# Performance work log

Hardware: AMD Instinct MI355X
Metric: run time of the kernel (lower is better)

The kernel has to match this reference:

```python
import jax, jax.numpy as jnp
import numpy as np

E = 768
H = 12
D = E // H  # 64


def setup_inputs() -> dict:
    key = jax.random.key(0)
    ks = jax.random.split(key, 12)
    B, S = 4, 2048
    scale = 1.0 / np.sqrt(E)
    inp = {
        "q": jax.random.normal(ks[0], (B, S, E), jnp.float32),
        "k": jax.random.normal(ks[1], (B, S, E), jnp.float32),
        "v": jax.random.normal(ks[2], (B, S, E), jnp.float32),
        "mask": jax.random.randint(ks[3], (B, S), 0, 2, jnp.int32),
        "Wq": jax.random.normal(ks[4], (E, E), jnp.float32) * scale,
        "bq": jnp.zeros((E,), jnp.float32),
        "Wk": jax.random.normal(ks[5], (E, E), jnp.float32) * scale,
        "bk": jnp.zeros((E,), jnp.float32),
        "Wv": jax.random.normal(ks[6], (E, E), jnp.float32) * scale,
        "bv": jnp.zeros((E,), jnp.float32),
        "Wo": jax.random.normal(ks[7], (E, E), jnp.float32) * scale,
        "bo": jnp.zeros((E,), jnp.float32),
    }
    return inp


def reference(q, k, v, mask, Wq, bq, Wk, bk, Wv, bv, Wo, bo):
    B, Sq, _ = q.shape
    Sk = k.shape[1]
    # QKV projections, split into heads: [B, H, S, D]
    qh = (q @ Wq + bq).reshape(B, Sq, H, D).transpose(0, 2, 1, 3)
    kh = (k @ Wk + bk).reshape(B, Sk, H, D).transpose(0, 2, 1, 3)
    vh = (v @ Wv + bv).reshape(B, Sk, H, D).transpose(0, 2, 1, 3)
    scores = jnp.einsum("bhqd,bhkd->bhqk", qh, kh) / jnp.sqrt(jnp.float32(D))
    # enc=True padding-mask path: positions where mask==0 get -1e9 added
    bias = jnp.where(mask == 0, jnp.float32(-1e9), jnp.float32(0.0))  # [B, Sk]
    scores = scores + bias[:, None, None, :]
    weights = jax.nn.softmax(scores, axis=-1)
    # dropout is identity in eval mode
    ctx = jnp.einsum("bhqk,bhkd->bqhd", weights, vh).reshape(B, Sq, E)
    return ctx @ Wo + bo
```

## Files before the change

kernel.cpp:

```cpp
#include <hip/hip_runtime.h>
#include <hip/hip_bf16.h>
#include <stdint.h>


typedef __bf16 bf16x8 __attribute__((ext_vector_type(8)));
typedef __bf16 bf16x4 __attribute__((ext_vector_type(4)));
typedef float floatx4 __attribute__((ext_vector_type(4)));

#define MFMA_BF16(a, b, c) __builtin_amdgcn_mfma_f32_16x16x32_bf16(a, b, c, 0, 0, 0)


__device__ __forceinline__ void glds16(const __bf16* g, __bf16* l) {
  __builtin_amdgcn_global_load_lds(
      (const __attribute__((address_space(1))) unsigned int*)g,
      (__attribute__((address_space(3))) unsigned int*)l, 16, 0, 0);
}

__global__ __launch_bounds__(256) void prep_transpose(
    const float* __restrict__ W0, const float* __restrict__ W1,
    const float* __restrict__ W2, const float* __restrict__ W3,
    __bf16* __restrict__ T0, __bf16* __restrict__ T1,
    __bf16* __restrict__ T2, __bf16* __restrict__ T3) {
  const int z = blockIdx.z;
  const float* W = (z == 0) ? W0 : (z == 1) ? W1 : (z == 2) ? W2 : W3;
  __bf16* T = (z == 0) ? T0 : (z == 1) ? T1 : (z == 2) ? T2 : T3;
  __shared__ float t[32][33];
  const int tx = threadIdx.x & 31, ty = threadIdx.x >> 5;
  const int kb = blockIdx.x * 32, nb = blockIdx.y * 32;
#pragma unroll
  for (int j = 0; j < 4; ++j)
    t[ty + j * 8][tx] = W[(size_t)(kb + ty + j * 8) * 768 + nb + tx];
  __syncthreads();
#pragma unroll
  for (int j = 0; j < 4; ++j)
    T[(size_t)(nb + ty + j * 8) * 768 + kb + tx] = (__bf16)t[tx][ty + j * 8];
}

__global__ __launch_bounds__(256) void qkv_gemm(
    const __bf16* __restrict__ Wtq, const __bf16* __restrict__ Wtk,
    const __bf16* __restrict__ Wtv, const float* __restrict__ Xq,
    const float* __restrict__ Xk, const float* __restrict__ Xv,
    const float* __restrict__ bq, const float* __restrict__ bk,
    const float* __restrict__ bv, __bf16* __restrict__ Qh,
    __bf16* __restrict__ Kh, __bf16* __restrict__ Vt) {
  __shared__ __align__(16) __bf16 As[128 * 32];
  __shared__ __align__(16) __bf16 Bs[128 * 32];
  const int gid = blockIdx.x + 6 * blockIdx.y + 384 * blockIdx.z;
  const int swz = (gid & 7) * 144 + (gid >> 3);
  const int z = swz / 384;
  const int rem = swz - z * 384;
  const int by = rem / 6;
  const int bx = rem - by * 6;

  const __bf16* Aop = (z == 0) ? Wtq : (z == 1) ? Wtk : Wtv;
  const float* Bop = (z == 0) ? Xq : (z == 1) ? Xk : Xv;
  const float* bias = (z == 0) ? bq : (z == 1) ? bk : bv;
  __bf16* Dst = (z == 0) ? Qh : (z == 1) ? Kh : Vt;
  const int m0 = bx * 128, n0 = by * 128;

  const int tid = threadIdx.x, lane = tid & 63, w = tid >> 6;
  const int quad = lane >> 4, l16 = lane & 15;
  const int wm = (w >> 1) * 64, wn = (w & 1) * 64;

  const int garow = w * 32 + (lane >> 2);
  const int gacol = (lane & 3) * 8;
  const __bf16* gA = Aop + (size_t)(m0 + garow) * 768 + gacol;
  __bf16* lA = As + w * 1024;
  const int brow = tid >> 3, bcol = (tid & 7) * 4;

  floatx4 acc[4][4] = {};

  for (int k0 = 0; k0 < 768; k0 += 32) {
    __syncthreads();
    glds16(gA, lA);
    glds16(gA + (size_t)16 * 768, lA + 512);
    gA += 32;
    float4 f[4];
#pragma unroll
    for (int j = 0; j < 4; ++j)
      f[j] = *(const float4*)&Bop[(size_t)(n0 + brow + 32 * j) * 768 + k0 + bcol];
#pragma unroll
    for (int j = 0; j < 4; ++j) {
      bf16x4 pv;
      pv[0] = (__bf16)f[j].x; pv[1] = (__bf16)f[j].y;
      pv[2] = (__bf16)f[j].z; pv[3] = (__bf16)f[j].w;
      *(bf16x4*)&Bs[(brow + 32 * j) * 32 + bcol] = pv;
    }
    __syncthreads();
    bf16x8 af[4], bfr[4];
#pragma unroll
    for (int t = 0; t < 4; ++t) {
      af[t] = *(const bf16x8*)&As[(wm + t * 16 + l16) * 32 + quad * 8];
      bfr[t] = *(const bf16x8*)&Bs[(wn + t * 16 + l16) * 32 + quad * 8];
    }
#pragma unroll
    for (int mt = 0; mt < 4; ++mt)
#pragma unroll
      for (int nt = 0; nt < 4; ++nt)
        acc[mt][nt] = MFMA_BF16(af[mt], bfr[nt], acc[mt][nt]);
  }

#pragma unroll
  for (int mt = 0; mt < 4; ++mt) {
    const int e = m0 + wm + mt * 16 + quad * 4;
    const float4 b4 = *(const float4*)&bias[e];
    const int h = e >> 6, d = e & 63;
#pragma unroll
    for (int nt = 0; nt < 4; ++nt) {
      const int s = n0 + wn + nt * 16 + l16;
      const int bb = s >> 11, sr = s & 2047;
      const float v0 = acc[mt][nt][0] + b4.x;
      const float v1 = acc[mt][nt][1] + b4.y;
      const float v2 = acc[mt][nt][2] + b4.z;
      const float v3 = acc[mt][nt][3] + b4.w;
      if (z < 2) {
        bf16x4 pv;
        pv[0] = (__bf16)v0; pv[1] = (__bf16)v1; pv[2] = (__bf16)v2; pv[3] = (__bf16)v3;
        const int col = (z == 0) ? d : ((((d >> 3) ^ (sr & 7)) << 3) | (d & 7));
        *(bf16x4*)&Dst[((size_t)(bb * 12 + h) * 2048 + sr) * 64 + col] = pv;
      } else {
        const size_t rowbase = ((size_t)(bb * 12 + h) * 64 + d) * 2048;
        const int shi = sr & ~63, sblk = (sr >> 3) & 7, soff = sr & 7;
        Dst[rowbase + 0 * 2048 + shi + (((sblk ^ ((d + 0) & 7))) << 3) + soff] = (__bf16)v0;
        Dst[rowbase + 1 * 2048 + shi + (((sblk ^ ((d + 1) & 7))) << 3) + soff] = (__bf16)v1;
        Dst[rowbase + 2 * 2048 + shi + (((sblk ^ ((d + 2) & 7))) << 3) + soff] = (__bf16)v2;
        Dst[rowbase + 3 * 2048 + shi + (((sblk ^ ((d + 3) & 7))) << 3) + soff] = (__bf16)v3;
      }
    }
  }
}

__global__ __launch_bounds__(256) void out_gemm(const __bf16* __restrict__ Wto,
                                                const __bf16* __restrict__ Ctx,
                                                const float* __restrict__ bo,
                                                float* __restrict__ Out) {
  __shared__ __align__(16) __bf16 As[128 * 32];
  __shared__ __align__(16) __bf16 Bs[128 * 32];
  const int gid = blockIdx.x + 6 * blockIdx.y;
  const int swz = (gid & 7) * 48 + (gid >> 3);
  const int by = swz / 6;
  const int bx = swz - by * 6;
  const int m0 = bx * 128, n0 = by * 128;
  const int tid = threadIdx.x, lane = tid & 63, w = tid >> 6;
  const int quad = lane >> 4, l16 = lane & 15;
  const int wm = (w >> 1) * 64, wn = (w & 1) * 64;

  const int grow = w * 32 + (lane >> 2);
  const int gcol = (lane & 3) * 8;
  const __bf16* gA = Wto + (size_t)(m0 + grow) * 768 + gcol;
  const __bf16* gB = Ctx + (size_t)(n0 + grow) * 768 + gcol;
  __bf16* lA = As + w * 1024;
  __bf16* lB = Bs + w * 1024;

  floatx4 acc[4][4] = {};
  for (int k0 = 0; k0 < 768; k0 += 32) {
    __syncthreads();
    glds16(gA, lA);
    glds16(gA + (size_t)16 * 768, lA + 512);
    glds16(gB, lB);
    glds16(gB + (size_t)16 * 768, lB + 512);
    gA += 32;
    gB += 32;
    __syncthreads();
    bf16x8 af[4], bfr[4];
#pragma unroll
    for (int t = 0; t < 4; ++t) {
      af[t] = *(const bf16x8*)&As[(wm + t * 16 + l16) * 32 + quad * 8];
      bfr[t] = *(const bf16x8*)&Bs[(wn + t * 16 + l16) * 32 + quad * 8];
    }
#pragma unroll
    for (int mt = 0; mt < 4; ++mt)
#pragma unroll
      for (int nt = 0; nt < 4; ++nt)
        acc[mt][nt] = MFMA_BF16(af[mt], bfr[nt], acc[mt][nt]);
  }

#pragma unroll
  for (int mt = 0; mt < 4; ++mt) {
    const int e = m0 + wm + mt * 16 + quad * 4;
    const float4 b4 = *(const float4*)&bo[e];
#pragma unroll
    for (int nt = 0; nt < 4; ++nt) {
      const int s = n0 + wn + nt * 16 + l16;
      float4 r;
      r.x = acc[mt][nt][0] + b4.x;
      r.y = acc[mt][nt][1] + b4.y;
      r.z = acc[mt][nt][2] + b4.z;
      r.w = acc[mt][nt][3] + b4.w;
      *(float4*)&Out[(size_t)s * 768 + e] = r;
    }
  }
}

__global__ __launch_bounds__(256) void attn_kernel(
    const __bf16* __restrict__ Qh, const __bf16* __restrict__ Kh,
    const __bf16* __restrict__ Vt, const int* __restrict__ mask,
    __bf16* __restrict__ ctx) {
  const int lid = blockIdx.x + 16 * blockIdx.y;
  const int swz = (lid & 7) * 96 + (lid >> 3);
  const int qx = swz & 15, bh = swz >> 4;
  const int b = bh / 12, h = bh - b * 12;
  const int tid = threadIdx.x, lane = tid & 63, w = tid >> 6;
  const int quad = lane >> 4, l16 = lane & 15;
  const int q0 = qx * 128 + w * 32;

  __shared__ __align__(16) __bf16 Ks[2][64 * 64];
  __shared__ __align__(16) __bf16 Vs[2][64 * 64];
  __shared__ __align__(16) __bf16 Plds[4][32][72];

  const __bf16* Qbase = Qh + (size_t)bh * 2048 * 64;
  const __bf16* Kbase = Kh + (size_t)bh * 2048 * 64;
  const __bf16* Vbase = Vt + (size_t)bh * 64 * 2048;
  const int* maskB = mask + b * 2048;

  bf16x8 bqf[2][2];
#pragma unroll
  for (int qt = 0; qt < 2; ++qt)
#pragma unroll
    for (int c = 0; c < 2; ++c)
      bqf[qt][c] =
          *(const bf16x8*)&Qbase[(size_t)(q0 + qt * 16 + l16) * 64 + c * 32 + quad * 8];

  const int r0 = (w * 2) * 8 + (lane >> 3);
  const int r1 = (w * 2 + 1) * 8 + (lane >> 3);
  const int scol = (lane & 7) * 8;
  const int d0 = (w * 2) * 512;
  const int d1 = (w * 2 + 1) * 512;
  const int col0 = (quad ^ (l16 & 7)) * 8;

  glds16(&Kbase[(size_t)r0 * 64 + scol], &Ks[0][d0]);
  glds16(&Kbase[(size_t)r1 * 64 + scol], &Ks[0][d1]);
  glds16(&Vbase[(size_t)r0 * 2048 + scol], &Vs[0][d0]);
  glds16(&Vbase[(size_t)r1 * 2048 + scol], &Vs[0][d1]);

  floatx4 o[4][2] = {};
  float rS[2] = {0.0f, 0.0f};
  const float SC = 0.18033688011112042f;

  for (int it = 0; it < 32; ++it) {
    const int kt = it * 64;
    const int cur = it & 1;
    const int nxt = cur ^ 1;
    const int nkt = (kt + 64) & 2047;

    __syncthreads();

    glds16(&Kbase[(size_t)(nkt + r0) * 64 + scol], &Ks[nxt][d0]);
    glds16(&Kbase[(size_t)(nkt + r1) * 64 + scol], &Ks[nxt][d1]);
    glds16(&Vbase[(size_t)r0 * 2048 + nkt + scol], &Vs[nxt][d0]);
    glds16(&Vbase[(size_t)r1 * 2048 + nkt + scol], &Vs[nxt][d1]);

    int4 mk[4];
#pragma unroll
    for (int t = 0; t < 4; ++t) mk[t] = *(const int4*)&maskB[kt + t * 16 + quad * 4];

    floatx4 sc[4][2];
#pragma unroll
    for (int t = 0; t < 4; ++t) {
      bf16x8 ak0 = *(const bf16x8*)&Ks[cur][(t * 16 + l16) * 64 + col0];
      bf16x8 ak1 = *(const bf16x8*)&Ks[cur][(t * 16 + l16) * 64 + (col0 ^ 32)];
#pragma unroll
      for (int qt = 0; qt < 2; ++qt) {
        floatx4 zz = {};
        zz = MFMA_BF16(ak0, bqf[qt][0], zz);
        zz = MFMA_BF16(ak1, bqf[qt][1], zz);
        sc[t][qt] = zz;
      }
    }
#pragma unroll
    for (int t = 0; t < 4; ++t) {
      const float k0f = mk[t].x ? 0.0f : -1e5f;
      const float k1f = mk[t].y ? 0.0f : -1e5f;
      const float k2f = mk[t].z ? 0.0f : -1e5f;
      const float k3f = mk[t].w ? 0.0f : -1e5f;
#pragma unroll
      for (int qt = 0; qt < 2; ++qt) {
        floatx4 p;
        p[0] = __builtin_amdgcn_exp2f(fmaf(sc[t][qt][0], SC, k0f));
        p[1] = __builtin_amdgcn_exp2f(fmaf(sc[t][qt][1], SC, k1f));
        p[2] = __builtin_amdgcn_exp2f(fmaf(sc[t][qt][2], SC, k2f));
        p[3] = __builtin_amdgcn_exp2f(fmaf(sc[t][qt][3], SC, k3f));
        sc[t][qt] = p;
        rS[qt] += p[0] + p[1] + p[2] + p[3];
      }
    }
#pragma unroll
    for (int qt = 0; qt < 2; ++qt)
#pragma unroll
      for (int t = 0; t < 4; ++t) {
        bf16x4 pv;
        pv[0] = (__bf16)sc[t][qt][0];
        pv[1] = (__bf16)sc[t][qt][1];
        pv[2] = (__bf16)sc[t][qt][2];
        pv[3] = (__bf16)sc[t][qt][3];
        *(bf16x4*)&Plds[w][qt * 16 + l16][t * 16 + quad * 4] = pv;
      }
#pragma unroll
    for (int c = 0; c < 2; ++c) {
      bf16x8 bp[2];
#pragma unroll
      for (int qt = 0; qt < 2; ++qt)
        bp[qt] = *(const bf16x8*)&Plds[w][qt * 16 + l16][c * 32 + quad * 8];
#pragma unroll
      for (int dt = 0; dt < 4; ++dt) {
        bf16x8 av = *(const bf16x8*)&Vs[cur][(dt * 16 + l16) * 64 + (col0 ^ (c * 32))];
#pragma unroll
        for (int qt = 0; qt < 2; ++qt) o[dt][qt] = MFMA_BF16(av, bp[qt], o[dt][qt]);
      }
    }
  }

  float inv[2];
#pragma unroll
  for (int qt = 0; qt < 2; ++qt) {
    float s = rS[qt];
    s += __shfl_xor(s, 16, 64);
    s += __shfl_xor(s, 32, 64);
    inv[qt] = 1.0f / s;
  }
#pragma unroll
  for (int dt = 0; dt < 4; ++dt)
#pragma unroll
    for (int qt = 0; qt < 2; ++qt) {
      const int q = q0 + qt * 16 + l16;
      const int d = h * 64 + dt * 16 + quad * 4;
      bf16x4 pv;
      pv[0] = (__bf16)(o[dt][qt][0] * inv[qt]);
      pv[1] = (__bf16)(o[dt][qt][1] * inv[qt]);
      pv[2] = (__bf16)(o[dt][qt][2] * inv[qt]);
      pv[3] = (__bf16)(o[dt][qt][3] * inv[qt]);
      *(bf16x4*)&ctx[(size_t)(b * 2048 + q) * 768 + d] = pv;
    }
}

extern "C" void kernel_launch(void* const* d_in, const int* in_sizes, int n_in,
                              void* d_out, int out_size, void* d_ws, size_t ws_size,
                              hipStream_t stream) {
  const float* q = (const float*)d_in[0];
  const float* k = (const float*)d_in[1];
  const float* v = (const float*)d_in[2];
  const int* mask = (const int*)d_in[3];
  const float* Wq = (const float*)d_in[4];
  const float* bq = (const float*)d_in[5];
  const float* Wk = (const float*)d_in[6];
  const float* bk = (const float*)d_in[7];
  const float* Wv = (const float*)d_in[8];
  const float* bv = (const float*)d_in[9];
  const float* Wo = (const float*)d_in[10];
  const float* bo = (const float*)d_in[11];
  float* out = (float*)d_out;

  char* ws = (char*)d_ws;
  const size_t SZ = (size_t)8192 * 768 * 2;
  const size_t WSZ = (size_t)768 * 768 * 2;
  __bf16* Qh = (__bf16*)(ws);
  __bf16* Kh = (__bf16*)(ws + SZ);
  __bf16* Vt = (__bf16*)(ws + 2 * SZ);
  __bf16* ctx = (__bf16*)(ws + 3 * SZ);
  __bf16* Wtq = (__bf16*)(ws + 4 * SZ);
  __bf16* Wtk = (__bf16*)(ws + 4 * SZ + WSZ);
  __bf16* Wtv = (__bf16*)(ws + 4 * SZ + 2 * WSZ);
  __bf16* Wto = (__bf16*)(ws + 4 * SZ + 3 * WSZ);

  prep_transpose<<<dim3(24, 24, 4), 256, 0, stream>>>(Wq, Wk, Wv, Wo, Wtq, Wtk, Wtv, Wto);
  qkv_gemm<<<dim3(6, 64, 3), 256, 0, stream>>>(Wtq, Wtk, Wtv, q, k, v, bq, bk, bv,
                                               Qh, Kh, Vt);
  attn_kernel<<<dim3(16, 48), 256, 0, stream>>>(Qh, Kh, Vt, mask, ctx);
  out_gemm<<<dim3(6, 64), 256, 0, stream>>>(Wto, ctx, bo, out);
}
```

Baseline: 298.4 us.

## Keep softmax probabilities in registers via permlane swaps, fold scale and mask bias

The attention kernel no longer round-trips the probability tile through LDS. It reorders bf16 P fragments across lanes with permlane32/16 swaps and computes row sums with an extra MFMA against a ones vector. The softmax scale is folded into the Q projection epilogue, and the padding mask is precomputed as a float bias that seeds the QK MFMA accumulator, which removes per-element FMAs and selects. This adds a small mask-to-bias pass in the prep kernel and relies on gfx950 permlane swap instructions and inline asm bf16 packing.

```diff
diff --git a/kernel.cpp b/kernel.cpp
--- a/kernel.cpp
+++ b/kernel.cpp
@@ -16,11 +16,36 @@
       (__attribute__((address_space(3))) unsigned int*)l, 16, 0, 0);
 }
 
+#if __has_builtin(__builtin_amdgcn_permlane32_swap)
+__device__ __forceinline__ void perm32_swap(unsigned int& a, unsigned int& b) {
+  auto r = __builtin_amdgcn_permlane32_swap(a, b, false, false);
+  a = r[0];
+  b = r[1];
+}
+#else
+__device__ __forceinline__ void perm32_swap(unsigned int& a, unsigned int& b) {
+  asm("v_permlane32_swap_b32 %0, %1" : "+v"(a), "+v"(b));
+}
+#endif
+
+#if __has_builtin(__builtin_amdgcn_permlane16_swap)
+__device__ __forceinline__ void perm16_swap(unsigned int& a, unsigned int& b) {
+  auto r = __builtin_amdgcn_permlane16_swap(a, b, false, false);
+  a = r[0];
+  b = r[1];
+}
+#else
+__device__ __forceinline__ void perm16_swap(unsigned int& a, unsigned int& b) {
+  asm("v_permlane16_swap_b32 %0, %1" : "+v"(a), "+v"(b));
+}
+#endif
+
 __global__ __launch_bounds__(256) void prep_transpose(
     const float* __restrict__ W0, const float* __restrict__ W1,
     const float* __restrict__ W2, const float* __restrict__ W3,
     __bf16* __restrict__ T0, __bf16* __restrict__ T1,
-    __bf16* __restrict__ T2, __bf16* __restrict__ T3) {
+    __bf16* __restrict__ T2, __bf16* __restrict__ T3,
+    const int* __restrict__ mask, float* __restrict__ biasF) {
   const int z = blockIdx.z;
   const float* W = (z == 0) ? W0 : (z == 1) ? W1 : (z == 2) ? W2 : W3;
   __bf16* T = (z == 0) ? T0 : (z == 1) ? T1 : (z == 2) ? T2 : T3;
@@ -30,6 +55,16 @@
 #pragma unroll
   for (int j = 0; j < 4; ++j)
     t[ty + j * 8][tx] = W[(size_t)(kb + ty + j * 8) * 768 + nb + tx];
+  if (z == 3 && blockIdx.y == 0 && blockIdx.x < 8) {
+    const int idx = blockIdx.x * 1024 + threadIdx.x * 4;
+    const int4 m4 = *(const int4*)&mask[idx];
+    float4 f4;
+    f4.x = m4.x ? 0.0f : -1e5f;
+    f4.y = m4.y ? 0.0f : -1e5f;
+    f4.z = m4.z ? 0.0f : -1e5f;
+    f4.w = m4.w ? 0.0f : -1e5f;
+    *(float4*)&biasF[idx] = f4;
+  }
   __syncthreads();
 #pragma unroll
   for (int j = 0; j < 4; ++j)
@@ -100,6 +135,7 @@
         acc[mt][nt] = MFMA_BF16(af[mt], bfr[nt], acc[mt][nt]);
   }
 
+  const float qs = (z == 0) ? 0.18033688011112042f : 1.0f;
 #pragma unroll
   for (int mt = 0; mt < 4; ++mt) {
     const int e = m0 + wm + mt * 16 + quad * 4;
@@ -109,10 +145,10 @@
     for (int nt = 0; nt < 4; ++nt) {
       const int s = n0 + wn + nt * 16 + l16;
       const int bb = s >> 11, sr = s & 2047;
-      const float v0 = acc[mt][nt][0] + b4.x;
-      const float v1 = acc[mt][nt][1] + b4.y;
-      const float v2 = acc[mt][nt][2] + b4.z;
-      const float v3 = acc[mt][nt][3] + b4.w;
+      const float v0 = (acc[mt][nt][0] + b4.x) * qs;
+      const float v1 = (acc[mt][nt][1] + b4.y) * qs;
+      const float v2 = (acc[mt][nt][2] + b4.z) * qs;
+      const float v3 = (acc[mt][nt][3] + b4.w) * qs;
       if (z < 2) {
         bf16x4 pv;
         pv[0] = (__bf16)v0; pv[1] = (__bf16)v1; pv[2] = (__bf16)v2; pv[3] = (__bf16)v3;
@@ -194,7 +230,7 @@
 
 __global__ __launch_bounds__(256) void attn_kernel(
     const __bf16* __restrict__ Qh, const __bf16* __restrict__ Kh,
-    const __bf16* __restrict__ Vt, const int* __restrict__ mask,
+    const __bf16* __restrict__ Vt, const float* __restrict__ biasF,
     __bf16* __restrict__ ctx) {
   const int lid = blockIdx.x + 16 * blockIdx.y;
   const int swz = (lid & 7) * 96 + (lid >> 3);
@@ -206,12 +242,11 @@
 
   __shared__ __align__(16) __bf16 Ks[2][64 * 64];
   __shared__ __align__(16) __bf16 Vs[2][64 * 64];
-  __shared__ __align__(16) __bf16 Plds[4][32][72];
 
   const __bf16* Qbase = Qh + (size_t)bh * 2048 * 64;
   const __bf16* Kbase = Kh + (size_t)bh * 2048 * 64;
   const __bf16* Vbase = Vt + (size_t)bh * 64 * 2048;
-  const int* maskB = mask + b * 2048;
+  const float* biasB = biasF + b * 2048;
 
   bf16x8 bqf[2][2];
 #pragma unroll
@@ -234,8 +269,10 @@
   glds16(&Vbase[(size_t)r1 * 2048 + scol], &Vs[0][d1]);
 
   floatx4 o[4][2] = {};
-  float rS[2] = {0.0f, 0.0f};
-  const float SC = 0.18033688011112042f;
+  floatx4 os[2] = {};
+  bf16x8 ones8;
+#pragma unroll
+  for (int j = 0; j < 8; ++j) ones8[j] = (__bf16)1.0f;
 
   for (int it = 0; it < 32; ++it) {
     const int kt = it * 64;
@@ -250,57 +287,49 @@
     glds16(&Vbase[(size_t)r0 * 2048 + nkt + scol], &Vs[nxt][d0]);
     glds16(&Vbase[(size_t)r1 * 2048 + nkt + scol], &Vs[nxt][d1]);
 
-    int4 mk[4];
-#pragma unroll
-    for (int t = 0; t < 4; ++t) mk[t] = *(const int4*)&maskB[kt + t * 16 + quad * 4];
-
     floatx4 sc[4][2];
 #pragma unroll
     for (int t = 0; t < 4; ++t) {
+      const float4 bf4 = *(const float4*)&biasB[kt + t * 16 + quad * 4];
       bf16x8 ak0 = *(const bf16x8*)&Ks[cur][(t * 16 + l16) * 64 + col0];
       bf16x8 ak1 = *(const bf16x8*)&Ks[cur][(t * 16 + l16) * 64 + (col0 ^ 32)];
 #pragma unroll
       for (int qt = 0; qt < 2; ++qt) {
-        floatx4 zz = {};
+        floatx4 zz;
+        zz[0] = bf4.x; zz[1] = bf4.y; zz[2] = bf4.z; zz[3] = bf4.w;
         zz = MFMA_BF16(ak0, bqf[qt][0], zz);
         zz = MFMA_BF16(ak1, bqf[qt][1], zz);
         sc[t][qt] = zz;
       }
     }
-#pragma unroll
-    for (int t = 0; t < 4; ++t) {
-      const float k0f = mk[t].x ? 0.0f : -1e5f;
-      const float k1f = mk[t].y ? 0.0f : -1e5f;
-      const float k2f = mk[t].z ? 0.0f : -1e5f;
-      const float k3f = mk[t].w ? 0.0f : -1e5f;
+    unsigned int u[4][2][2];
+#pragma unroll
+    for (int t = 0; t < 4; ++t)
 #pragma unroll
       for (int qt = 0; qt < 2; ++qt) {
-        floatx4 p;
-        p[0] = __builtin_amdgcn_exp2f(fmaf(sc[t][qt][0], SC, k0f));
-        p[1] = __builtin_amdgcn_exp2f(fmaf(sc[t][qt][1], SC, k1f));
-        p[2] = __builtin_amdgcn_exp2f(fmaf(sc[t][qt][2], SC, k2f));
-        p[3] = __builtin_amdgcn_exp2f(fmaf(sc[t][qt][3], SC, k3f));
-        sc[t][qt] = p;
-        rS[qt] += p[0] + p[1] + p[2] + p[3];
-      }
-    }
-#pragma unroll
-    for (int qt = 0; qt < 2; ++qt)
-#pragma unroll
-      for (int t = 0; t < 4; ++t) {
-        bf16x4 pv;
-        pv[0] = (__bf16)sc[t][qt][0];
-        pv[1] = (__bf16)sc[t][qt][1];
-        pv[2] = (__bf16)sc[t][qt][2];
-        pv[3] = (__bf16)sc[t][qt][3];
-        *(bf16x4*)&Plds[w][qt * 16 + l16][t * 16 + quad * 4] = pv;
+        const float e0 = __builtin_amdgcn_exp2f(sc[t][qt][0]);
+        const float e1 = __builtin_amdgcn_exp2f(sc[t][qt][1]);
+        const float e2 = __builtin_amdgcn_exp2f(sc[t][qt][2]);
+        const float e3 = __builtin_amdgcn_exp2f(sc[t][qt][3]);
+        asm("v_cvt_pk_bf16_f32 %0, %1, %2" : "=v"(u[t][qt][0]) : "v"(e0), "v"(e1));
+        asm("v_cvt_pk_bf16_f32 %0, %1, %2" : "=v"(u[t][qt][1]) : "v"(e2), "v"(e3));
       }
 #pragma unroll
     for (int c = 0; c < 2; ++c) {
       bf16x8 bp[2];
 #pragma unroll
-      for (int qt = 0; qt < 2; ++qt)
-        bp[qt] = *(const bf16x8*)&Plds[w][qt * 16 + l16][c * 32 + quad * 8];
+      for (int qt = 0; qt < 2; ++qt) {
+        unsigned int w0 = u[2 * c][qt][0], w1 = u[2 * c][qt][1];
+        unsigned int w2 = u[2 * c + 1][qt][0], w3 = u[2 * c + 1][qt][1];
+        perm32_swap(w0, w2);
+        perm32_swap(w1, w3);
+        perm16_swap(w0, w2);
+        perm16_swap(w1, w3);
+        union { unsigned int wd[4]; bf16x8 v; } ub;
+        ub.wd[0] = w0; ub.wd[1] = w1; ub.wd[2] = w2; ub.wd[3] = w3;
+        bp[qt] = ub.v;
+        os[qt] = MFMA_BF16(ones8, bp[qt], os[qt]);
+      }
 #pragma unroll
       for (int dt = 0; dt < 4; ++dt) {
         bf16x8 av = *(const bf16x8*)&Vs[cur][(dt * 16 + l16) * 64 + (col0 ^ (c * 32))];
@@ -311,13 +340,8 @@
   }
 
   float inv[2];
-#pragma unroll
-  for (int qt = 0; qt < 2; ++qt) {
-    float s = rS[qt];
-    s += __shfl_xor(s, 16, 64);
-    s += __shfl_xor(s, 32, 64);
-    inv[qt] = 1.0f / s;
-  }
+  inv[0] = 1.0f / os[0][0];
+  inv[1] = 1.0f / os[1][0];
 #pragma unroll
   for (int dt = 0; dt < 4; ++dt)
 #pragma unroll
@@ -361,10 +385,12 @@
   __bf16* Wtk = (__bf16*)(ws + 4 * SZ + WSZ);
   __bf16* Wtv = (__bf16*)(ws + 4 * SZ + 2 * WSZ);
   __bf16* Wto = (__bf16*)(ws + 4 * SZ + 3 * WSZ);
-
-  prep_transpose<<<dim3(24, 24, 4), 256, 0, stream>>>(Wq, Wk, Wv, Wo, Wtq, Wtk, Wtv, Wto);
+  float* biasF = (float*)(ws + 4 * SZ + 4 * WSZ);
+
+  prep_transpose<<<dim3(24, 24, 4), 256, 0, stream>>>(Wq, Wk, Wv, Wo, Wtq, Wtk,
+                                                      Wtv, Wto, mask, biasF);
   qkv_gemm<<<dim3(6, 64, 3), 256, 0, stream>>>(Wtq, Wtk, Wtv, q, k, v, bq, bk, bv,
                                                Qh, Kh, Vt);
-  attn_kernel<<<dim3(16, 48), 256, 0, stream>>>(Qh, Kh, Vt, mask, ctx);
+  attn_kernel<<<dim3(16, 48), 256, 0, stream>>>(Qh, Kh, Vt, biasF, ctx);
   out_gemm<<<dim3(6, 64), 256, 0, stream>>>(Wto, ctx, bo, out);
 }
```

Result: faster. 280.6 us (-6.0%).
